# Performance work log

Hardware: AMD Instinct MI355X
Metric: run time of the kernel (lower is better)

The kernel has to match this reference:

```python
import jax, jax.numpy as jnp
import numpy as np

B, S, D = 4, 2048, 1024
NB_HEAD, SIZE_PER_HEAD = 16, 64  # output_dim = 1024


def setup_inputs() -> dict:
    key = jax.random.key(0)
    ks = jax.random.split(key, 6)
    out_dim = NB_HEAD * SIZE_PER_HEAD
    return {
        "q_seq": jax.random.normal(ks[0], (B, S, D), dtype=jnp.float32),
        "k_seq": jax.random.normal(ks[1], (B, S, D), dtype=jnp.float32),
        "v_seq": jax.random.normal(ks[2], (B, S, D), dtype=jnp.float32),
        "WQ": jax.random.normal(ks[3], (D, out_dim), dtype=jnp.float32) * (1.0 / np.sqrt(D)),
        "WK": jax.random.normal(ks[4], (D, out_dim), dtype=jnp.float32) * (1.0 / np.sqrt(D)),
        "WV": jax.random.normal(ks[5], (D, out_dim), dtype=jnp.float32) * (1.0 / np.sqrt(D)),
    }


def reference(q_seq, k_seq, v_seq, WQ, WK, WV):
    h, dh = NB_HEAD, SIZE_PER_HEAD
    b, sq, _ = q_seq.shape
    sk = k_seq.shape[1]
    # QKV projections, then split heads: [b, s, h*dh] -> [b, h, s, dh]
    Q = (q_seq @ WQ).reshape(b, sq, h, dh).transpose(0, 2, 1, 3)
    Kp = (k_seq @ WK).reshape(b, sk, h, dh).transpose(0, 2, 1, 3)
    V = (v_seq @ WV).reshape(b, sk, h, dh).transpose(0, 2, 1, 3)
    scale = 1.0 / jnp.sqrt(jnp.asarray(dh, dtype=Q.dtype))
    # scores [b, h, q, k]; V_len is None so no additive mask is applied
    A = jnp.einsum("bhqd,bhkd->bhqk", Q, Kp) * scale
    A = jax.nn.softmax(A, axis=-1)
    O = jnp.einsum("bhqk,bhkd->bhqd", A, V)
    # merge heads back: [b, q, h*dh]; Q_len is None so no mul-mask
    return O.transpose(0, 2, 1, 3).reshape(b, sq, h * dh)
```

## Files before the change

### kernel.cpp

```cpp
#include <hip/hip_runtime.h>
#include <hip/hip_bf16.h>
#include <stdint.h>

#define B_ 4
#define S_ 2048
#define D_ 1024
#define H_ 16
#define DH_ 64
#define BH_ 64
#define M_ 8192

typedef __bf16 bf16;
typedef __attribute__((ext_vector_type(4))) __bf16 bf16x4;
typedef __attribute__((ext_vector_type(8))) __bf16 bf16x8;
typedef __attribute__((ext_vector_type(4))) float f32x4;
typedef __attribute__((ext_vector_type(8))) float f32x8;

#define EXP2F(x) __builtin_amdgcn_exp2f(x)

__device__ inline void gload16(const void* g, void* l) {
  __builtin_amdgcn_global_load_lds((const __attribute__((address_space(1))) void*)g,
                                   (__attribute__((address_space(3))) void*)l, 16, 0, 0);
}

__global__ __launch_bounds__(256) void k_wt(const float* __restrict__ wq,
    const float* __restrict__ wk, const float* __restrict__ wv, bf16* __restrict__ o) {
  __shared__ float t[32][132];
  int z = blockIdx.z;
  const float* w = z == 0 ? wq : (z == 1 ? wk : wv);
  bf16* d = o + (size_t)z * D_ * D_;
  int bn = blockIdx.x * 128;
  int bk = blockIdx.y * 32;
  int tid = threadIdx.x;
  int lc = (tid & 31) * 4, lk = tid >> 5;
#pragma unroll
  for (int j = 0; j < 4; j++) {
    f32x4 v = *(const f32x4*)&w[(size_t)(bk + lk + 8 * j) * D_ + bn + lc];
    *(f32x4*)&t[lk + 8 * j][lc] = v;
  }
  __syncthreads();
  int c = tid >> 1, kh = (tid & 1) * 16;
  bf16x8 r0, r1;
#pragma unroll
  for (int j = 0; j < 8; j++) {
    r0[j] = (bf16)t[kh + j][c];
    r1[j] = (bf16)t[kh + 8 + j][c];
  }
  *(bf16x8*)&d[(size_t)(bn + c) * D_ + bk + kh] = r0;
  *(bf16x8*)&d[(size_t)(bn + c) * D_ + bk + kh + 8] = r1;
}

__global__ __launch_bounds__(256) void k_proj(const float* __restrict__ Xq,
    const float* __restrict__ Xk, const float* __restrict__ Xv,
    const bf16* __restrict__ WT, bf16* __restrict__ Qo, bf16* __restrict__ Ko,
    bf16* __restrict__ VTo) {
  __shared__ char lds[49152];
  int z = blockIdx.z;
  const float* Xz = z == 0 ? Xq : (z == 1 ? Xk : Xv);
  const char* Ab = (const char*)Xz;
  const char* Bb = (const char*)(WT + (size_t)z * D_ * D_);
  int m0 = blockIdx.x * 128, n0 = blockIdx.y * 128;
  int tid = threadIdx.x, lane = tid & 63, w = tid >> 6;
  int wr = w >> 1, wc = w & 1, fr = lane & 15, fg = lane >> 4;
  f32x4 acc[4][4];
#pragma unroll
  for (int a = 0; a < 4; a++)
#pragma unroll
    for (int b = 0; b < 4; b++) acc[a][b] = (f32x4){0.f, 0.f, 0.f, 0.f};

  for (int k0 = 0; k0 < D_; k0 += 64) {
#pragma unroll
    for (int it = 0; it < 12; ++it) {
      int ow = (w + 4 * it) * 1024;
      int o = ow + lane * 16;
      const char* src;
      if (o < 32768) {
        int row = o >> 8;
        int db = (o & 255) ^ ((row & 15) << 4);
        src = Ab + (size_t)(m0 + row) * 4096 + k0 * 4 + db;
      } else {
        int lo = o - 32768, row = lo >> 7;
        int db = (lo & 127) ^ ((row & 7) << 4);
        src = Bb + (size_t)(n0 + row) * 2048 + k0 * 2 + db;
      }
      gload16(src, (char*)lds + ow);
    }
    __syncthreads();
#pragma unroll
    for (int c = 0; c < 2; c++) {
      bf16x8 af[4], bfr[4];
#pragma unroll
      for (int mi = 0; mi < 4; mi++) {
        int row = wr * 64 + mi * 16 + fr;
        int kb = fg * 32 + 128 * c;
        int sx = (row & 15) << 4;
        f32x4 a0 = *(const f32x4*)(lds + row * 256 + (kb ^ sx));
        f32x4 a1 = *(const f32x4*)(lds + row * 256 + ((kb + 16) ^ sx));
        bf16x8 v;
#pragma unroll
        for (int j = 0; j < 4; j++) { v[j] = (bf16)a0[j]; v[4 + j] = (bf16)a1[j]; }
        af[mi] = v;
      }
#pragma unroll
      for (int ni = 0; ni < 4; ni++) {
        int row = wc * 64 + ni * 16 + fr;
        bfr[ni] = *(const bf16x8*)(lds + 32768 + row * 128 +
                                   ((fg * 16 + 64 * c) ^ ((row & 7) << 4)));
      }
#pragma unroll
      for (int mi = 0; mi < 4; mi++)
#pragma unroll
        for (int ni = 0; ni < 4; ni++)
          acc[mi][ni] = __builtin_amdgcn_mfma_f32_16x16x32_bf16(af[mi], bfr[ni],
                                                                acc[mi][ni], 0, 0, 0);
    }
    __syncthreads();
  }
  if (z == 2) {
#pragma unroll
    for (int mi = 0; mi < 4; mi++) {
      int row = m0 + wr * 64 + mi * 16 + 4 * fg;
      int bI = row >> 11, s = row & 2047;
      int blk = s >> 6, kk = s & 63;
      int slot = (kk & 0x23) | ((kk & 0x0C) << 1) | ((kk & 0x10) >> 2);
#pragma unroll
      for (int ni = 0; ni < 4; ni++) {
        int col = n0 + wc * 64 + ni * 16 + fr;
        int h = col >> 6, d = col & 63;
        bf16x4 vv = (bf16x4){(bf16)acc[mi][ni][0], (bf16)acc[mi][ni][1],
                             (bf16)acc[mi][ni][2], (bf16)acc[mi][ni][3]};
        *(bf16x4*)&VTo[((size_t)(bI * H_ + h) * DH_ + d) * S_ + blk * 64 + slot] = vv;
      }
    }
  } else {
    bf16* O = z == 0 ? Qo : Ko;
    float sc = (z == 0) ? 0.18033688011112042f : 1.0f;
#pragma unroll
    for (int mi = 0; mi < 4; mi++)
#pragma unroll
      for (int r = 0; r < 4; r++) {
        int row = m0 + wr * 64 + mi * 16 + 4 * fg + r;
        int b = row >> 11, s = row & 2047;
#pragma unroll
        for (int ni = 0; ni < 4; ni++) {
          int col = n0 + wc * 64 + ni * 16 + fr;
          int h = col >> 6, d = col & 63;
          O[((size_t)(b * H_ + h) * S_ + s) * DH_ + d] = (bf16)(acc[mi][ni][r] * sc);
        }
      }
  }
}

__global__ __launch_bounds__(512, 4) void k_attn(const bf16* __restrict__ Q,
    const bf16* __restrict__ Kt, const bf16* __restrict__ VT, float* __restrict__ out) {
  __shared__ bf16 kv[16384];
  int g = blockIdx.x;
  int wg = (g & 7) * 64 + (g >> 3);
  int qt = wg & 7, bh = wg >> 3;
  int b = bh >> 4, h = bh & 15;
  int tid = threadIdx.x, lane = tid & 63, w = tid >> 6;
  int fr = lane & 15, fg = lane >> 4;
  const char* Kb = (const char*)(Kt + (size_t)bh * S_ * DH_);
  const char* Vb = (const char*)(VT + (size_t)bh * DH_ * S_);
  int q0 = qt * 256 + w * 32;

  int o0 = tid * 16;
  int r0 = o0 >> 7, b0 = (o0 & 127) ^ ((r0 & 7) << 4);
  const char* kp = Kb + r0 * 128 + b0;
  const char* vp = Vb + r0 * 4096 + b0;
  char* lb = (char*)kv;
  int w1024 = w * 1024;

  const int swz = (fr & 7) << 3;
  const bf16* kb0 = &kv[fr * 64 + ((fg * 8) ^ swz)];
  const bf16* kb1 = &kv[fr * 64 + ((fg * 8 + 32) ^ swz)];
  const bf16* vb0 = kb0 + 4096;
  const bf16* vb1 = kb1 + 4096;

  bf16x8 qf[2][2];
#pragma unroll
  for (int mi = 0; mi < 2; mi++)
#pragma unroll
    for (int c = 0; c < 2; c++)
      qf[mi][c] = *(const bf16x8*)(Q + ((size_t)bh * S_ + q0 + mi * 16 + fr) * DH_ + fg * 8 + 32 * c);
  float m_[2] = {-1e30f, -1e30f};
  f32x4 o_[2][4];
#pragma unroll
  for (int mi = 0; mi < 2; mi++)
#pragma unroll
    for (int ds = 0; ds < 4; ds++) o_[mi][ds] = (f32x4){0.f, 0.f, 0.f, 0.f};
  f32x4 ol[2] = {(f32x4){0.f, 0.f, 0.f, 0.f}, (f32x4){0.f, 0.f, 0.f, 0.f}};
  bf16x8 vones;
#pragma unroll
  for (int j = 0; j < 8; j++) vones[j] = (bf16)1.0f;

  gload16(kp, lb + w1024);
  gload16(vp, lb + 8192 + w1024);
  kp += 8192; vp += 128;

#pragma unroll 2
  for (int kt = 0; kt < 32; ++kt) {
    __syncthreads();
    if (kt + 1 < 32) {
      const int nb = ((kt + 1) & 1) << 14;
      gload16(kp, lb + nb + w1024);
      gload16(vp, lb + nb + 8192 + w1024);
      kp += 8192; vp += 128;
    }
    const int cb = (kt & 1) << 13;
    f32x4 st[2][4];
    __builtin_amdgcn_s_setprio(1);
#pragma unroll
    for (int ks = 0; ks < 4; ks++) {
      bf16x8 kf0 = *(const bf16x8*)(kb0 + cb + ks * 1024);
      bf16x8 kf1 = *(const bf16x8*)(kb1 + cb + ks * 1024);
#pragma unroll
      for (int mi = 0; mi < 2; mi++) {
        f32x4 a = (f32x4){0.f, 0.f, 0.f, 0.f};
        a = __builtin_amdgcn_mfma_f32_16x16x32_bf16(kf0, qf[mi][0], a, 0, 0, 0);
        a = __builtin_amdgcn_mfma_f32_16x16x32_bf16(kf1, qf[mi][1], a, 0, 0, 0);
        st[mi][ks] = a;
      }
    }
    __builtin_amdgcn_s_setprio(0);
    bf16x8 pa[2][2];
#pragma unroll
    for (int mi = 0; mi < 2; mi++) {
      float ma = fmaxf(fmaxf(st[mi][0][0], st[mi][0][1]), st[mi][0][2]);
      float mb = fmaxf(fmaxf(st[mi][0][3], st[mi][1][0]), st[mi][1][1]);
      float mc = fmaxf(fmaxf(st[mi][1][2], st[mi][1][3]), st[mi][2][0]);
      float md = fmaxf(fmaxf(st[mi][2][1], st[mi][2][2]), st[mi][2][3]);
      float me = fmaxf(fmaxf(st[mi][3][0], st[mi][3][1]), st[mi][3][2]);
      float mx = fmaxf(fmaxf(fmaxf(ma, mb), mc), fmaxf(fmaxf(md, me), st[mi][3][3]));
      mx = fmaxf(mx, __shfl_xor(mx, 16));
      mx = fmaxf(mx, __shfl_xor(mx, 32));
      if (!__all(mx - m_[mi] <= 7.0f)) {
        float mnew = fmaxf(m_[mi], mx);
        float sf = EXP2F(m_[mi] - mnew);
        m_[mi] = mnew;
        float s0 = __shfl(sf, 4 * fg + 0);
        float s1 = __shfl(sf, 4 * fg + 1);
        float s2 = __shfl(sf, 4 * fg + 2);
        float s3 = __shfl(sf, 4 * fg + 3);
#pragma unroll
        for (int ds = 0; ds < 4; ds++) {
          o_[mi][ds][0] *= s0; o_[mi][ds][1] *= s1;
          o_[mi][ds][2] *= s2; o_[mi][ds][3] *= s3;
        }
        ol[mi][0] *= s0; ol[mi][1] *= s1; ol[mi][2] *= s2; ol[mi][3] *= s3;
      }
#pragma unroll
      for (int ks = 0; ks < 4; ks++)
#pragma unroll
        for (int r = 0; r < 4; r++) st[mi][ks][r] = EXP2F(st[mi][ks][r] - m_[mi]);
      pa[mi][0] = (bf16x8){(bf16)st[mi][0][0], (bf16)st[mi][0][1], (bf16)st[mi][0][2],
                           (bf16)st[mi][0][3], (bf16)st[mi][1][0], (bf16)st[mi][1][1],
                           (bf16)st[mi][1][2], (bf16)st[mi][1][3]};
      pa[mi][1] = (bf16x8){(bf16)st[mi][2][0], (bf16)st[mi][2][1], (bf16)st[mi][2][2],
                           (bf16)st[mi][2][3], (bf16)st[mi][3][0], (bf16)st[mi][3][1],
                           (bf16)st[mi][3][2], (bf16)st[mi][3][3]};
    }
    __builtin_amdgcn_s_setprio(1);
#pragma unroll
    for (int mi = 0; mi < 2; mi++) {
      ol[mi] = __builtin_amdgcn_mfma_f32_16x16x32_bf16(pa[mi][0], vones, ol[mi], 0, 0, 0);
      ol[mi] = __builtin_amdgcn_mfma_f32_16x16x32_bf16(pa[mi][1], vones, ol[mi], 0, 0, 0);
    }
#pragma unroll
    for (int c = 0; c < 2; c++) {
      const bf16* vbc = c ? vb1 : vb0;
#pragma unroll
      for (int ds = 0; ds < 4; ds++) {
        bf16x8 vf = *(const bf16x8*)(vbc + cb + ds * 1024);
        o_[0][ds] = __builtin_amdgcn_mfma_f32_16x16x32_bf16(pa[0][c], vf, o_[0][ds], 0, 0, 0);
        o_[1][ds] = __builtin_amdgcn_mfma_f32_16x16x32_bf16(pa[1][c], vf, o_[1][ds], 0, 0, 0);
      }
    }
    __builtin_amdgcn_s_setprio(0);
  }
#pragma unroll
  for (int mi = 0; mi < 2; mi++)
#pragma unroll
    for (int r = 0; r < 4; r++) {
      float inv = 1.0f / ol[mi][r];
      int s = q0 + mi * 16 + 4 * fg + r;
#pragma unroll
      for (int ds = 0; ds < 4; ds++) {
        int col = h * DH_ + ds * 16 + fr;
        out[((size_t)b * S_ + s) * D_ + col] = o_[mi][ds][r] * inv;
      }
    }
}

extern "C" void kernel_launch(void* const* d_in, const int* in_sizes, int n_in,
                              void* d_out, int out_size, void* d_ws, size_t ws_size,
                              hipStream_t stream) {
  (void)in_sizes; (void)n_in; (void)out_size; (void)ws_size;
  const float* q  = (const float*)d_in[0];
  const float* k  = (const float*)d_in[1];
  const float* v  = (const float*)d_in[2];
  const float* wq = (const float*)d_in[3];
  const float* wk = (const float*)d_in[4];
  const float* wv = (const float*)d_in[5];
  float* out = (float*)d_out;
  char* ws = (char*)d_ws;
  size_t off = 0;
  bf16* wt = (bf16*)(ws + off); off += (size_t)3 * D_ * D_ * 2;
  bf16* Qw = (bf16*)(ws + off); off += (size_t)BH_ * S_ * DH_ * 2;
  bf16* Kw = (bf16*)(ws + off); off += (size_t)BH_ * S_ * DH_ * 2;
  bf16* Vt = (bf16*)(ws + off); off += (size_t)BH_ * S_ * DH_ * 2;

  k_wt  <<<dim3(8, 32, 3), 256, 0, stream>>>(wq, wk, wv, wt);
  k_proj<<<dim3(64, 8, 3), 256, 0, stream>>>(q, k, v, wt, Qw, Kw, Vt);
  k_attn<<<dim3(512), 512, 0, stream>>>(Qw, Kw, Vt, out);
}
```

Measured before the change: 161.1 us.

## Double-buffer projection GEMM LDS and widen tiles to 128x256 with 512 threads

```diff
diff --git a/kernel.cpp b/kernel.cpp
--- a/kernel.cpp
+++ b/kernel.cpp
@@ -50,42 +50,67 @@
   *(bf16x8*)&d[(size_t)(bn + c) * D_ + bk + kh + 8] = r1;
 }
 
-__global__ __launch_bounds__(256) void k_proj(const float* __restrict__ Xq,
+__global__ __launch_bounds__(512, 2) void k_proj(const float* __restrict__ Xq,
     const float* __restrict__ Xk, const float* __restrict__ Xv,
     const bf16* __restrict__ WT, bf16* __restrict__ Qo, bf16* __restrict__ Ko,
     bf16* __restrict__ VTo) {
-  __shared__ char lds[49152];
+  __shared__ char lds[131072];
   int z = blockIdx.z;
   const float* Xz = z == 0 ? Xq : (z == 1 ? Xk : Xv);
   const char* Ab = (const char*)Xz;
   const char* Bb = (const char*)(WT + (size_t)z * D_ * D_);
-  int m0 = blockIdx.x * 128, n0 = blockIdx.y * 128;
+  int m0 = blockIdx.x * 128, n0 = blockIdx.y * 256;
   int tid = threadIdx.x, lane = tid & 63, w = tid >> 6;
-  int wr = w >> 1, wc = w & 1, fr = lane & 15, fg = lane >> 4;
+  int wr = w >> 2, wc = w & 3, fr = lane & 15, fg = lane >> 4;
   f32x4 acc[4][4];
 #pragma unroll
   for (int a = 0; a < 4; a++)
 #pragma unroll
     for (int b = 0; b < 4; b++) acc[a][b] = (f32x4){0.f, 0.f, 0.f, 0.f};
 
-  for (int k0 = 0; k0 < D_; k0 += 64) {
-#pragma unroll
-    for (int it = 0; it < 12; ++it) {
-      int ow = (w + 4 * it) * 1024;
-      int o = ow + lane * 16;
-      const char* src;
-      if (o < 32768) {
-        int row = o >> 8;
-        int db = (o & 255) ^ ((row & 15) << 4);
-        src = Ab + (size_t)(m0 + row) * 4096 + k0 * 4 + db;
-      } else {
-        int lo = o - 32768, row = lo >> 7;
-        int db = (lo & 127) ^ ((row & 7) << 4);
-        src = Bb + (size_t)(n0 + row) * 2048 + k0 * 2 + db;
-      }
-      gload16(src, (char*)lds + ow);
-    }
+  int w1024 = w * 1024;
+
+#pragma unroll
+  for (int it = 0; it < 8; ++it) {
+    int ow = (w + 8 * it) * 1024;
+    int o = ow + lane * 16;
+    const char* src;
+    if (o < 32768) {
+      int row = o >> 8;
+      int db = (o & 255) ^ ((row & 15) << 4);
+      src = Ab + (size_t)(m0 + row) * 4096 + db;
+    } else {
+      int lo = o - 32768, row = lo >> 7;
+      int db = (lo & 127) ^ ((row & 7) << 4);
+      src = Bb + (size_t)(n0 + row) * 2048 + db;
+    }
+    gload16(src, lds + ow);
+  }
+
+#pragma unroll 2
+  for (int t = 0; t < 16; ++t) {
     __syncthreads();
+    if (t + 1 < 16) {
+      const int nb = ((t + 1) & 1) << 16;
+      const int k0 = (t + 1) * 64;
+#pragma unroll
+      for (int it = 0; it < 8; ++it) {
+        int ow = (w + 8 * it) * 1024;
+        int o = ow + lane * 16;
+        const char* src;
+        if (o < 32768) {
+          int row = o >> 8;
+          int db = (o & 255) ^ ((row & 15) << 4);
+          src = Ab + (size_t)(m0 + row) * 4096 + k0 * 4 + db;
+        } else {
+          int lo = o - 32768, row = lo >> 7;
+          int db = (lo & 127) ^ ((row & 7) << 4);
+          src = Bb + (size_t)(n0 + row) * 2048 + k0 * 2 + db;
+        }
+        gload16(src, lds + nb + ow);
+      }
+    }
+    const int cb = (t & 1) << 16;
 #pragma unroll
     for (int c = 0; c < 2; c++) {
       bf16x8 af[4], bfr[4];
@@ -94,8 +119,8 @@
         int row = wr * 64 + mi * 16 + fr;
         int kb = fg * 32 + 128 * c;
         int sx = (row & 15) << 4;
-        f32x4 a0 = *(const f32x4*)(lds + row * 256 + (kb ^ sx));
-        f32x4 a1 = *(const f32x4*)(lds + row * 256 + ((kb + 16) ^ sx));
+        f32x4 a0 = *(const f32x4*)(lds + cb + row * 256 + (kb ^ sx));
+        f32x4 a1 = *(const f32x4*)(lds + cb + row * 256 + ((kb + 16) ^ sx));
         bf16x8 v;
 #pragma unroll
         for (int j = 0; j < 4; j++) { v[j] = (bf16)a0[j]; v[4 + j] = (bf16)a1[j]; }
@@ -104,7 +129,7 @@
 #pragma unroll
       for (int ni = 0; ni < 4; ni++) {
         int row = wc * 64 + ni * 16 + fr;
-        bfr[ni] = *(const bf16x8*)(lds + 32768 + row * 128 +
+        bfr[ni] = *(const bf16x8*)(lds + cb + 32768 + row * 128 +
                                    ((fg * 16 + 64 * c) ^ ((row & 7) << 4)));
       }
 #pragma unroll
@@ -114,7 +139,6 @@
           acc[mi][ni] = __builtin_amdgcn_mfma_f32_16x16x32_bf16(af[mi], bfr[ni],
                                                                 acc[mi][ni], 0, 0, 0);
     }
-    __syncthreads();
   }
   if (z == 2) {
 #pragma unroll
@@ -311,6 +335,6 @@
   bf16* Vt = (bf16*)(ws + off); off += (size_t)BH_ * S_ * DH_ * 2;
 
   k_wt  <<<dim3(8, 32, 3), 256, 0, stream>>>(wq, wk, wv, wt);
-  k_proj<<<dim3(64, 8, 3), 256, 0, stream>>>(q, k, v, wt, Qw, Kw, Vt);
+  k_proj<<<dim3(64, 4, 3), 512, 0, stream>>>(q, k, v, wt, Qw, Kw, Vt);
   k_attn<<<dim3(512), 512, 0, stream>>>(Qw, Kw, Vt, out);
 }
```

Result: faster. 155.9 us (-3.2%).
